# Performance work log

Hardware: AMD Instinct MI355X
Metric: run time of the kernel (lower is better)

## Reference

```python
import jax, jax.numpy as jnp
import numpy as np

T, B, E, H = 512, 64, 512, 1024


def setup_inputs() -> dict:
    key = jax.random.key(0)
    ks = jax.random.split(key, 14)
    s = 1.0 / np.sqrt(H)
    u = lambda k, shape: jax.random.uniform(k, shape, jnp.float32, -s, s)
    inp = {
        "embeds": jax.random.normal(ks[0], (T, B, E), jnp.float32),
        "Wgx": u(ks[1], (H, E)), "Wgh": u(ks[2], (H, H)), "bg": u(ks[3], (H, 1)),
        "Wix": u(ks[4], (H, E)), "Wih": u(ks[5], (H, H)), "bi": u(ks[6], (H, 1)),
        "Wfx": u(ks[7], (H, E)), "Wfh": u(ks[8], (H, H)), "bf": u(ks[9], (H, 1)) + 1.0,
        "Wox": u(ks[10], (H, E)), "Woh": u(ks[11], (H, H)), "bo": u(ks[12], (H, 1)),
    }
    return inp


def reference(embeds, Wgx, Wgh, bg, Wix, Wih, bi, Wfx, Wfh, bf, Wox, Woh, bo):
    # embeds: [T, B, E]. Faithful to the original (buggy) module:
    #   prev_c is never updated (stays 0), and prev_h is overwritten with c,
    #   so the recurrent carry is c_{t-1} and c_t = g_t * i_t.
    t_, b_, _ = embeds.shape
    h_ = Wgx.shape[0]
    # Precompute input projections for all timesteps: [T, H, B]
    xg = jnp.einsum('he,tbe->thb', Wgx, embeds) + bg
    xi = jnp.einsum('he,tbe->thb', Wix, embeds) + bi
    xf = jnp.einsum('he,tbe->thb', Wfx, embeds) + bf
    xo = jnp.einsum('he,tbe->thb', Wox, embeds) + bo

    def step(prev_h, xs):
        xg_t, xi_t, xf_t, xo_t = xs
        g = jnp.tanh(xg_t + Wgh @ prev_h)
        i = jax.nn.sigmoid(xi_t + Wih @ prev_h)
        f = jax.nn.sigmoid(xf_t + Wfh @ prev_h)  # multiplies prev_c == 0
        o = jax.nn.sigmoid(xo_t + Woh @ prev_h)
        c = g * i + 0.0 * f  # prev_c stays zero in the original
        h = jnp.tanh(c) * o
        return c, h.T  # bug: carry becomes c, output h is [B, H]

    prev_h0 = jnp.zeros((h_, b_), embeds.dtype)
    _, hiddens = jax.lax.scan(step, prev_h0, (xg, xi, xf, xo))
    return hiddens  # [T, B, H]
```

## Files before the change

### kernel.cpp

```cpp
#include <hip/hip_runtime.h>
#include <stdint.h>


#define T_ 512
#define B_ 64
#define E_ 512
#define H_ 1024
#define QS ((size_t)T_ * B_ * H_)
#define ROWF ((size_t)(B_ * H_))
#define CH_OFF (ROWF / 2)

typedef short bf16x8 __attribute__((ext_vector_type(8)));
typedef float f32x4  __attribute__((ext_vector_type(4)));
typedef float f32x16 __attribute__((ext_vector_type(16)));

__device__ __forceinline__ unsigned int f2bf(float f) {
    unsigned int u = __builtin_bit_cast(unsigned int, f);
    return (u + 0x7fffu + ((u >> 16) & 1u)) >> 16;
}
__device__ __forceinline__ float bf2f(unsigned int s) {
    unsigned int u = (s & 0xffffu) << 16;
    return __builtin_bit_cast(float, u);
}
__device__ __forceinline__ float fsigm(float x) { return 1.f / (1.f + __expf(-x)); }
__device__ __forceinline__ float ftanh(float x) { float e = __expf(2.f * x); return 1.f - 2.f / (e + 1.f); }

__device__ __forceinline__ unsigned ldflag(const unsigned* p) {
    return __hip_atomic_load(p, __ATOMIC_RELAXED, __HIP_MEMORY_SCOPE_AGENT);
}
__device__ __forceinline__ void stflag(unsigned* p, unsigned v) {
    __hip_atomic_store(p, v, __ATOMIC_RELAXED, __HIP_MEMORY_SCOPE_AGENT);
}
__device__ __forceinline__ void st_ag64(void* p, unsigned long long v) {
    __hip_atomic_store((unsigned long long*)p, v, __ATOMIC_RELAXED, __HIP_MEMORY_SCOPE_AGENT);
}
__device__ __forceinline__ unsigned long long pk4bf(float a, float b, float c, float d) {
    return (unsigned long long)(f2bf(a) | (f2bf(b) << 16)) |
           ((unsigned long long)(f2bf(c) | (f2bf(d) << 16)) << 32);
}

__global__ __launch_bounds__(256) void cast_w1(const float* __restrict__ wg,
                                               const float* __restrict__ wi,
                                               const float* __restrict__ wo,
                                               unsigned short* __restrict__ dst) {
    int idx = blockIdx.x * 256 + threadIdx.x;
    const int per = H_ * E_ / 4;
    int q = idx / per;
    int loc = (idx - q * per) * 4;
    const float* src = (q == 0) ? wg : (q == 1) ? wi : wo;
    float4 v = *(const float4*)(src + loc);
    uint2 p;
    p.x = f2bf(v.x) | (f2bf(v.y) << 16);
    p.y = f2bf(v.z) | (f2bf(v.w) << 16);
    *(uint2*)(dst + (size_t)idx * 4) = p;
}

__global__ __launch_bounds__(256) void gemm_x(const float* __restrict__ emb,
                                              const unsigned short* __restrict__ Wb1,
                                              const float* __restrict__ bg,
                                              const float* __restrict__ bi,
                                              const float* __restrict__ bo,
                                              unsigned short* __restrict__ X) {
    const int t   = blockIdx.x >> 3;
    const int hb  = (blockIdx.x & 7) << 7;
    const int tid = threadIdx.x;
    __shared__ unsigned short eb[B_ * E_];

    const float* et = emb + (size_t)t * (B_ * E_);
    #pragma unroll
    for (int it = 0; it < 32; ++it) {
        int F = (it * 256 + tid) * 4;
        int b = F >> 9, e = F & 511;
        float4 v = *(const float4*)(et + F);
        uint2 p;
        p.x = f2bf(v.x) | (f2bf(v.y) << 16);
        p.y = f2bf(v.z) | (f2bf(v.w) << 16);
        *(uint2*)((char*)eb + b * 1024 + ((e * 2) ^ ((b & 7) << 4))) = p;
    }
    __syncthreads();

    const int w = tid >> 6, l = tid & 63;
    const int l31 = l & 31, l5 = l >> 5;
    const int hw = hb + (w << 5);

    f32x16 acc[3][2];
    #pragma unroll
    for (int q = 0; q < 3; ++q)
        #pragma unroll
        for (int n = 0; n < 2; ++n)
            #pragma unroll
            for (int k = 0; k < 16; ++k) acc[q][n][k] = 0.f;

    const unsigned short* Ar0 = Wb1 + ((size_t)0 * H_ + hw + l31) * E_ + l5 * 8;
    const unsigned short* Ar1 = Wb1 + ((size_t)1 * H_ + hw + l31) * E_ + l5 * 8;
    const unsigned short* Ar2 = Wb1 + ((size_t)2 * H_ + hw + l31) * E_ + l5 * 8;

    for (int s = 0; s < 32; ++s) {
        int r0 = l31, r1 = 32 + l31;
        int c0 = (s * 32 + l5 * 16) ^ ((r0 & 7) << 4);
        int c1 = (s * 32 + l5 * 16) ^ ((r1 & 7) << 4);
        bf16x8 Bf0 = *(const bf16x8*)((const char*)eb + r0 * 1024 + c0);
        bf16x8 Bf1 = *(const bf16x8*)((const char*)eb + r1 * 1024 + c1);
        bf16x8 a0 = *(const bf16x8*)(Ar0 + s * 16);
        bf16x8 a1 = *(const bf16x8*)(Ar1 + s * 16);
        bf16x8 a2 = *(const bf16x8*)(Ar2 + s * 16);
        acc[0][0] = __builtin_amdgcn_mfma_f32_32x32x16_bf16(a0, Bf0, acc[0][0], 0, 0, 0);
        acc[0][1] = __builtin_amdgcn_mfma_f32_32x32x16_bf16(a0, Bf1, acc[0][1], 0, 0, 0);
        acc[1][0] = __builtin_amdgcn_mfma_f32_32x32x16_bf16(a1, Bf0, acc[1][0], 0, 0, 0);
        acc[1][1] = __builtin_amdgcn_mfma_f32_32x32x16_bf16(a1, Bf1, acc[1][1], 0, 0, 0);
        acc[2][0] = __builtin_amdgcn_mfma_f32_32x32x16_bf16(a2, Bf0, acc[2][0], 0, 0, 0);
        acc[2][1] = __builtin_amdgcn_mfma_f32_32x32x16_bf16(a2, Bf1, acc[2][1], 0, 0, 0);
    }

    const float* bias[3] = {bg, bi, bo};
    #pragma unroll
    for (int q = 0; q < 3; ++q) {
        #pragma unroll
        for (int g4 = 0; g4 < 4; ++g4) {
            int h = hw + g4 * 8 + l5 * 4;
            float4 bv = *(const float4*)(bias[q] + h);
            #pragma unroll
            for (int n = 0; n < 2; ++n) {
                float v0 = acc[q][n][g4 * 4 + 0] + bv.x;
                float v1 = acc[q][n][g4 * 4 + 1] + bv.y;
                float v2 = acc[q][n][g4 * 4 + 2] + bv.z;
                float v3 = acc[q][n][g4 * 4 + 3] + bv.w;
                uint2 p;
                p.x = f2bf(v0) | (f2bf(v1) << 16);
                p.y = f2bf(v2) | (f2bf(v3) << 16);
                size_t o = ((size_t)q * T_ + t) * (size_t)(B_ * H_) + (size_t)((n << 5) + l31) * H_ + h;
                *(uint2*)(X + o) = p;
            }
        }
    }
}

__global__ __launch_bounds__(512) void lstm_rec(const float* __restrict__ Wgh,
                                                const float* __restrict__ Wih,
                                                const float* __restrict__ Woh,
                                                const unsigned short* __restrict__ X,
                                                unsigned short* __restrict__ ch512,
                                                unsigned* __restrict__ aflags,
                                                unsigned* __restrict__ bflags,
                                                float* __restrict__ out) {
    const int bid = blockIdx.x;
    const bool isA = bid < 64;
    const int blk = isA ? bid : bid - 64;
    const int h0 = blk << 4;
    const int tid = threadIdx.x;
    const int w = tid >> 6, l = tid & 63;
    const int kh = w >> 2, bq = w & 3;
    const int l15 = l & 15, l4 = l >> 4;
    const int kbase = kh << 9;
    const int bcol = (bq << 4) + l15;
    const int hrow = h0 + (l4 << 2);

    __shared__ float red[4][2][64][4];

    bf16x8 Ag[16], Ai[16];
    {
        const float* r0 = (isA ? Wgh : Woh) + (size_t)(h0 + l15) * H_ + kbase + l4 * 8;
        #pragma unroll
        for (int s = 0; s < 16; ++s) {
            float4 u = *(const float4*)(r0 + s * 32);
            float4 v = *(const float4*)(r0 + s * 32 + 4);
            bf16x8 a;
            a[0] = (short)f2bf(u.x); a[1] = (short)f2bf(u.y); a[2] = (short)f2bf(u.z); a[3] = (short)f2bf(u.w);
            a[4] = (short)f2bf(v.x); a[5] = (short)f2bf(v.y); a[6] = (short)f2bf(v.z); a[7] = (short)f2bf(v.w);
            Ag[s] = a;
        }
        if (isA) {
            const float* r1 = Wih + (size_t)(h0 + l15) * H_ + kbase + l4 * 8;
            #pragma unroll
            for (int s = 0; s < 16; ++s) {
                float4 u = *(const float4*)(r1 + s * 32);
                float4 v = *(const float4*)(r1 + s * 32 + 4);
                bf16x8 a;
                a[0] = (short)f2bf(u.x); a[1] = (short)f2bf(u.y); a[2] = (short)f2bf(u.z); a[3] = (short)f2bf(u.w);
                a[4] = (short)f2bf(v.x); a[5] = (short)f2bf(v.y); a[6] = (short)f2bf(v.z); a[7] = (short)f2bf(v.w);
                Ai[s] = a;
            }
        }
    }

    if (isA) {
        for (int t = 0; t < T_; ++t) {
            uint2 pg = {0, 0}, pi = {0, 0};
            if (kh == 0) {
                size_t xb = ((size_t)t * B_ + bcol) * H_ + hrow;
                pg = *(const uint2*)(X + xb);
                pi = *(const uint2*)(X + xb + QS);
            }

            if (t > 0) {
                if (tid < 64) {
                    while (!__all((int)(ldflag(aflags + tid) >= (unsigned)t)))
                        __builtin_amdgcn_s_sleep(1);
                }
                __syncthreads();
            }

            f32x4 acc0 = {0.f, 0.f, 0.f, 0.f}, acc1 = {0.f, 0.f, 0.f, 0.f};
            if (t > 0) {
                const unsigned short* ct = (const unsigned short*)(out + (size_t)t * ROWF + CH_OFF);
                const unsigned short* bp = ct + (size_t)bcol * H_ + kbase + l4 * 8;
                #pragma unroll
                for (int cch = 0; cch < 2; ++cch) {
                    bf16x8 bfr[8];
                    #pragma unroll
                    for (int s = 0; s < 8; ++s) bfr[s] = *(const bf16x8*)(bp + (cch * 8 + s) * 32);
                    #pragma unroll
                    for (int s = 0; s < 8; ++s) {
                        acc0 = __builtin_amdgcn_mfma_f32_16x16x32_bf16(Ag[cch * 8 + s], bfr[s], acc0, 0, 0, 0);
                        acc1 = __builtin_amdgcn_mfma_f32_16x16x32_bf16(Ai[cch * 8 + s], bfr[s], acc1, 0, 0, 0);
                    }
                }
                if (kh == 1) {
                    *(f32x4*)&red[bq][0][l][0] = acc0;
                    *(f32x4*)&red[bq][1][l][0] = acc1;
                }
                __syncthreads();
                if (kh == 0) {
                    acc0 += *(const f32x4*)&red[bq][0][l][0];
                    acc1 += *(const f32x4*)&red[bq][1][l][0];
                }
            }

            if (kh == 0) {
                float g0 = ftanh(acc0[0] + bf2f(pg.x));
                float g1 = ftanh(acc0[1] + bf2f(pg.x >> 16));
                float g2 = ftanh(acc0[2] + bf2f(pg.y));
                float g3 = ftanh(acc0[3] + bf2f(pg.y >> 16));
                float i0 = fsigm(acc1[0] + bf2f(pi.x));
                float i1 = fsigm(acc1[1] + bf2f(pi.x >> 16));
                float i2 = fsigm(acc1[2] + bf2f(pi.y));
                float i3 = fsigm(acc1[3] + bf2f(pi.y >> 16));
                unsigned short* cn = (t == T_ - 1) ? ch512
                                   : (unsigned short*)(out + (size_t)(t + 1) * ROWF + CH_OFF);
                st_ag64(cn + (size_t)bcol * H_ + hrow, pk4bf(g0 * i0, g1 * i1, g2 * i2, g3 * i3));
            }

            asm volatile("s_waitcnt vmcnt(0)" ::: "memory");
            __syncthreads();
            if (tid == 0) stflag(aflags + blk, (unsigned)(t + 1));
        }
    } else {
        float4 o_prev = {0.f, 0.f, 0.f, 0.f};
        for (int t = 0; t < T_; ++t) {
            uint2 po = {0, 0};
            if (kh == 0) {
                size_t xb = ((size_t)t * B_ + bcol) * H_ + hrow;
                po = *(const uint2*)(X + xb + 2 * QS);
            }

            if (t > 0) {
                if (tid < 64) {
                    while (!__all((int)(ldflag(aflags + tid) >= (unsigned)t &&
                                        ldflag(bflags + tid) >= (unsigned)t)))
                        __builtin_amdgcn_s_sleep(1);
                }
                __syncthreads();
            }

            f32x4 acc0 = {0.f, 0.f, 0.f, 0.f};
            if (t > 0) {
                const unsigned short* ct = (const unsigned short*)(out + (size_t)t * ROWF + CH_OFF);
                const unsigned short* bp = ct + (size_t)bcol * H_ + kbase + l4 * 8;
                #pragma unroll
                for (int cch = 0; cch < 2; ++cch) {
                    bf16x8 bfr[8];
                    #pragma unroll
                    for (int s = 0; s < 8; ++s) bfr[s] = *(const bf16x8*)(bp + (cch * 8 + s) * 32);
                    #pragma unroll
                    for (int s = 0; s < 8; ++s)
                        acc0 = __builtin_amdgcn_mfma_f32_16x16x32_bf16(Ag[cch * 8 + s], bfr[s], acc0, 0, 0, 0);
                }
                if (kh == 1) *(f32x4*)&red[bq][0][l][0] = acc0;
                __syncthreads();
                if (kh == 0) {
                    acc0 += *(const f32x4*)&red[bq][0][l][0];
                    uint2 pc = *(const uint2*)(ct + (size_t)bcol * H_ + hrow);
                    float4 hv;
                    hv.x = ftanh(bf2f(pc.x)) * o_prev.x;
                    hv.y = ftanh(bf2f(pc.x >> 16)) * o_prev.y;
                    hv.z = ftanh(bf2f(pc.y)) * o_prev.z;
                    hv.w = ftanh(bf2f(pc.y >> 16)) * o_prev.w;
                    *(float4*)(out + ((size_t)(t - 1) * ROWF) + (size_t)bcol * H_ + hrow) = hv;
                }
            }
            if (kh == 0) {
                o_prev.x = fsigm(acc0[0] + bf2f(po.x));
                o_prev.y = fsigm(acc0[1] + bf2f(po.x >> 16));
                o_prev.z = fsigm(acc0[2] + bf2f(po.y));
                o_prev.w = fsigm(acc0[3] + bf2f(po.y >> 16));
            }

            __syncthreads();
            if (tid == 0) stflag(bflags + blk, (unsigned)(t + 1));
        }
        if (tid < 64) {
            while (!__all((int)(ldflag(aflags + tid) >= (unsigned)T_ &&
                                ldflag(bflags + tid) >= (unsigned)T_)))
                __builtin_amdgcn_s_sleep(1);
        }
        __syncthreads();
        if (kh == 0) {
            uint2 pc = *(const uint2*)(ch512 + (size_t)bcol * H_ + hrow);
            float4 hv;
            hv.x = ftanh(bf2f(pc.x)) * o_prev.x;
            hv.y = ftanh(bf2f(pc.x >> 16)) * o_prev.y;
            hv.z = ftanh(bf2f(pc.y)) * o_prev.z;
            hv.w = ftanh(bf2f(pc.y >> 16)) * o_prev.w;
            *(float4*)(out + (size_t)(T_ - 1) * ROWF + (size_t)bcol * H_ + hrow) = hv;
        }
    }
}

extern "C" void kernel_launch(void* const* d_in, const int* in_sizes, int n_in,
                              void* d_out, int out_size, void* d_ws, size_t ws_size,
                              hipStream_t stream) {
    const float* emb = (const float*)d_in[0];
    const float* Wgx = (const float*)d_in[1];
    const float* Wgh = (const float*)d_in[2];
    const float* bg  = (const float*)d_in[3];
    const float* Wix = (const float*)d_in[4];
    const float* Wih = (const float*)d_in[5];
    const float* bi  = (const float*)d_in[6];
    const float* Wox = (const float*)d_in[10];
    const float* Woh = (const float*)d_in[11];
    const float* bo  = (const float*)d_in[12];
    float* out = (float*)d_out;

    char* ws = (char*)d_ws;
    const size_t wb1_bytes = (size_t)3 * H_ * E_ * 2;
    const size_t x_bytes   = (size_t)3 * T_ * B_ * H_ * 2;
    const size_t c_bytes   = (size_t)B_ * H_ * 2;
    unsigned short* Wb1 = (unsigned short*)ws;
    unsigned short* X   = (unsigned short*)(ws + wb1_bytes);
    unsigned short* c512 = (unsigned short*)(ws + wb1_bytes + x_bytes);
    unsigned* aflags = (unsigned*)(ws + wb1_bytes + x_bytes + c_bytes);

    hipMemsetAsync(aflags, 0, 512, stream);
    cast_w1<<<1536, 256, 0, stream>>>(Wgx, Wix, Wox, Wb1);
    gemm_x<<<T_ * 8, 256, 0, stream>>>(emb, Wb1, bg, bi, bo, X);
    lstm_rec<<<128, 512, 0, stream>>>(Wgh, Wih, Woh, X, c512, aflags, aflags + 64, out);
}
```

Before: 4.010 ms.

## Replace all-to-all flag polling with a dedicated coordinator block and padded flags

Adds an extra block that gathers per-block step flags and publishes per-block go flags. Worker blocks then spin on a single flag instead of 64 lanes polling every peer's flag. Flags are padded to separate 128-byte lines so that polling and publishing do not contend on shared cache lines. This should cut contention and polling traffic in the per-timestep grid barrier, at the cost of an extra hop through the coordinator. It also removes the s_sleep backoff. The coordinator barrier ends up slightly stricter than before, because A blocks now also wait for the B flags.

After: 3.574 ms. 10.9% less time.

```diff
diff --git a/kernel.cpp b/kernel.cpp
--- a/kernel.cpp
+++ b/kernel.cpp
@@ -9,6 +9,7 @@
 #define QS ((size_t)T_ * B_ * H_)
 #define ROWF ((size_t)(B_ * H_))
 #define CH_OFF (ROWF / 2)
+#define FLAG_U 32
 
 typedef short bf16x8 __attribute__((ext_vector_type(8)));
 typedef float f32x4  __attribute__((ext_vector_type(4)));
@@ -140,20 +141,38 @@
                                                 const float* __restrict__ Woh,
                                                 const unsigned short* __restrict__ X,
                                                 unsigned short* __restrict__ ch512,
-                                                unsigned* __restrict__ aflags,
-                                                unsigned* __restrict__ bflags,
+                                                unsigned* __restrict__ flagbase,
                                                 float* __restrict__ out) {
+    unsigned* aflagp = flagbase;
+    unsigned* bflagp = flagbase + 64 * FLAG_U;
+    unsigned* gop    = flagbase + 128 * FLAG_U;
+
     const int bid = blockIdx.x;
-    const bool isA = bid < 64;
-    const int blk = isA ? bid : bid - 64;
+    const int tid = threadIdx.x;
+
+    if (bid == 0) {
+        if (tid < 64) {
+            for (int u = 1; u <= T_; ++u) {
+                while (!__all((int)(ldflag(aflagp + tid * FLAG_U) >= (unsigned)u))) {}
+                stflag(gop + tid * FLAG_U, (unsigned)u);
+                while (!__all((int)(ldflag(bflagp + tid * FLAG_U) >= (unsigned)u))) {}
+                stflag(gop + (64 + tid) * FLAG_U, (unsigned)u);
+            }
+        }
+        return;
+    }
+
+    const bool isA = bid <= 64;
+    const int blk = isA ? bid - 1 : bid - 65;
     const int h0 = blk << 4;
-    const int tid = threadIdx.x;
     const int w = tid >> 6, l = tid & 63;
     const int kh = w >> 2, bq = w & 3;
     const int l15 = l & 15, l4 = l >> 4;
     const int kbase = kh << 9;
     const int bcol = (bq << 4) + l15;
     const int hrow = h0 + (l4 << 2);
+    unsigned* myflag = (isA ? aflagp : bflagp) + blk * FLAG_U;
+    const unsigned* mygo = gop + (isA ? blk : 64 + blk) * FLAG_U;
 
     __shared__ float red[4][2][64][4];
 
@@ -193,10 +212,7 @@
             }
 
             if (t > 0) {
-                if (tid < 64) {
-                    while (!__all((int)(ldflag(aflags + tid) >= (unsigned)t)))
-                        __builtin_amdgcn_s_sleep(1);
-                }
+                if (tid == 0) { while (ldflag(mygo) < (unsigned)t) {} }
                 __syncthreads();
             }
 
@@ -242,7 +258,7 @@
 
             asm volatile("s_waitcnt vmcnt(0)" ::: "memory");
             __syncthreads();
-            if (tid == 0) stflag(aflags + blk, (unsigned)(t + 1));
+            if (tid == 0) stflag(myflag, (unsigned)(t + 1));
         }
     } else {
         float4 o_prev = {0.f, 0.f, 0.f, 0.f};
@@ -254,11 +270,7 @@
             }
 
             if (t > 0) {
-                if (tid < 64) {
-                    while (!__all((int)(ldflag(aflags + tid) >= (unsigned)t &&
-                                        ldflag(bflags + tid) >= (unsigned)t)))
-                        __builtin_amdgcn_s_sleep(1);
-                }
+                if (tid == 0) { while (ldflag(mygo) < (unsigned)t) {} }
                 __syncthreads();
             }
 
@@ -296,13 +308,9 @@
             }
 
             __syncthreads();
-            if (tid == 0) stflag(bflags + blk, (unsigned)(t + 1));
-        }
-        if (tid < 64) {
-            while (!__all((int)(ldflag(aflags + tid) >= (unsigned)T_ &&
-                                ldflag(bflags + tid) >= (unsigned)T_)))
-                __builtin_amdgcn_s_sleep(1);
-        }
+            if (tid == 0) stflag(myflag, (unsigned)(t + 1));
+        }
+        if (tid == 0) { while (ldflag(mygo) < (unsigned)T_) {} }
         __syncthreads();
         if (kh == 0) {
             uint2 pc = *(const uint2*)(ch512 + (size_t)bcol * H_ + hrow);
@@ -332,16 +340,17 @@
     float* out = (float*)d_out;
 
     char* ws = (char*)d_ws;
-    const size_t wb1_bytes = (size_t)3 * H_ * E_ * 2;
-    const size_t x_bytes   = (size_t)3 * T_ * B_ * H_ * 2;
-    const size_t c_bytes   = (size_t)B_ * H_ * 2;
+    const size_t wb1_bytes  = (size_t)3 * H_ * E_ * 2;
+    const size_t x_bytes    = (size_t)3 * T_ * B_ * H_ * 2;
+    const size_t c_bytes    = (size_t)B_ * H_ * 2;
+    const size_t flag_bytes = (size_t)(64 + 64 + 128) * FLAG_U * 4;
     unsigned short* Wb1 = (unsigned short*)ws;
     unsigned short* X   = (unsigned short*)(ws + wb1_bytes);
     unsigned short* c512 = (unsigned short*)(ws + wb1_bytes + x_bytes);
-    unsigned* aflags = (unsigned*)(ws + wb1_bytes + x_bytes + c_bytes);
-
-    hipMemsetAsync(aflags, 0, 512, stream);
+    unsigned* flagbase = (unsigned*)(ws + wb1_bytes + x_bytes + c_bytes);
+
+    hipMemsetAsync(flagbase, 0, flag_bytes, stream);
     cast_w1<<<1536, 256, 0, stream>>>(Wgx, Wix, Wox, Wb1);
     gemm_x<<<T_ * 8, 256, 0, stream>>>(emb, Wb1, bg, bi, bo, X);
-    lstm_rec<<<128, 512, 0, stream>>>(Wgh, Wih, Woh, X, c512, aflags, aflags + 64, out);
-}
+    lstm_rec<<<129, 512, 0, stream>>>(Wgh, Wih, Woh, X, c512, flagbase, out);
+}
```
